# Optimization experiments

Measured on AMD Instinct MI355X. Metric: run time of the kernel, lower is better.

## Reference

```python
import jax, jax.numpy as jnp
import numpy as np

N, MA, F, NF = 512, 64, 128, 16
UPDATE_RATIO = 0.1
DECAY = 1.0
EPS = 1e-12  # avoids NaN grad of sqrt at self-distance 0 (torch diagonal is masked out by exp anyway)


def setup_inputs() -> dict:
    key = jax.random.key(0)
    ks = jax.random.split(key, 8)
    z = jax.random.randint(ks[0], (N, MA), 0, 10, dtype=jnp.int64) if jax.config.jax_enable_x64 else jax.random.randint(ks[0], (N, MA), 0, 10, dtype=jnp.int32)
    # pad last few atoms of each molecule with -1 to exercise the mask
    z = z.at[:, MA - 8:].set(-1)
    r = jax.random.normal(ks[1], (N, MA, 3), dtype=jnp.float32) * 3.0
    h = jax.random.normal(ks[2], (N, MA, F), dtype=jnp.float32)
    distances = jnp.linspace(0.5, 6.0, NF, dtype=jnp.float32)
    widths = jax.random.uniform(ks[3], (NF,), dtype=jnp.float32) * 0.5 + 0.5  # keep sigma > 0
    din = F * (1 + NF)  # 2176
    W1 = jax.random.normal(ks[4], (din, 512), dtype=jnp.float32) * (1.0 / np.sqrt(din))
    b1 = jnp.zeros((512,), dtype=jnp.float32)
    W2 = jax.random.normal(ks[5], (512, F), dtype=jnp.float32) * (1.0 / np.sqrt(512.0))
    b2 = jnp.zeros((F,), dtype=jnp.float32)
    return {"z": z, "r": r, "h": h, "distances": distances, "widths": widths,
            "W1": W1, "b1": b1, "W2": W2, "b2": b2}


def reference(z, r, h, distances, widths, W1, b1, W2, b2):
    n, ma = z.shape
    nf = distances.shape[0]
    # pairwise distance: (n, ma, ma)
    dv = r[:, :, None, :] - r[:, None, :, :]
    d = jnp.sqrt(jnp.sum(dv * dv, axis=-1) + EPS)
    mu = distances.reshape(1, nf, 1, 1)
    sigma = widths.reshape(1, nf, 1, 1)
    mask1 = (z > -1).astype(h.dtype)                      # (n, ma)
    pair_mask = mask1[:, :, None] * mask1[:, None, :]     # (n, ma, ma)
    # Gaussian RBF scores, masked: (n, nf, ma, ma)
    w = pair_mask[:, None] * jnp.exp(-((d[:, None] - mu) ** 2) / sigma) * 5.0
    # aggregate neighbor features: (n, ma, nf, F) -> (n, ma, nf*F)
    u = jnp.einsum('nfab,nbc->nafc', w, h).reshape(n, ma, nf * h.shape[-1])
    v = jnp.concatenate([h, u], axis=2)                   # (n, ma, F*(1+nf))
    v = jax.nn.silu(v @ W1 + b1) @ W2 + b2                # MLP 'net'
    h_new = h + v * UPDATE_RATIO * DECAY * mask1[:, :, None]
    return (z, r, h_new)
```

## Files before the change

### kernel.cpp

```cpp
#include <hip/hip_runtime.h>

#define MA 64
#define F 128
#define NF 16
#define HID 512
#define LDUB 144
#define LDWB 144
#define LDT1B 1040
#define UB0 0
#define UB1 9216
#define WL0 18432
#define WL1 27648

typedef float  float4v __attribute__((ext_vector_type(4)));
typedef short  short8  __attribute__((ext_vector_type(8)));
typedef int    int8v   __attribute__((ext_vector_type(8)));

static __device__ __forceinline__ unsigned int pack2bf(float x, float y) {
    unsigned int a = __float_as_uint(x) + 0x8000u;
    unsigned int b = __float_as_uint(y) + 0x8000u;
    return __builtin_amdgcn_perm(b, a, 0x07060302u);
}
static __device__ __forceinline__ unsigned short f2bf1(float x) {
    return (unsigned short)((__float_as_uint(x) + 0x8000u) >> 16);
}
static __device__ __forceinline__ unsigned int pk4fp8(float a, float b, float c, float d) {
    int p = __builtin_amdgcn_cvt_pk_fp8_f32(a, b, 0, false);
    p = __builtin_amdgcn_cvt_pk_fp8_f32(c, d, p, true);
    return (unsigned int)p;
}

#define LGKM_BAR() do {                                        \
    asm volatile("s_waitcnt lgkmcnt(0)" ::: "memory");         \
    __builtin_amdgcn_s_barrier();                              \
    asm volatile("" ::: "memory");                             \
} while (0)

__global__ void pack_frags(const float* __restrict__ W1, const float* __restrict__ W2,
                           unsigned char* __restrict__ w1p, unsigned short* __restrict__ w2p) {
    int gid  = blockIdx.x * 4 + (threadIdx.x >> 6);
    int lane = threadIdx.x & 63;
    int arow = lane & 15;
    int kq   = lane >> 4;
    if (gid < 544) {
        int kt = gid >> 5, jt = gid & 31;
        const float* base = W1 + (size_t)(kt * 128 + kq * 32) * HID + jt * 16 + arow;
        unsigned int o[8];
        #pragma unroll
        for (int p = 0; p < 8; p++)
            o[p] = pk4fp8(base[(p * 4 + 0) * HID], base[(p * 4 + 1) * HID],
                          base[(p * 4 + 2) * HID], base[(p * 4 + 3) * HID]);
        unsigned char* dst = w1p + ((size_t)gid * 64 + lane) * 32;
        *(uint4*)dst        = (uint4){o[0], o[1], o[2], o[3]};
        *(uint4*)(dst + 16) = (uint4){o[4], o[5], o[6], o[7]};
    } else if (gid < 544 + 128) {
        int g2 = gid - 544;
        int kt = g2 >> 3, mt = g2 & 7;
        const float* base = W2 + (size_t)(kt * 32 + kq * 8) * F + mt * 16 + arow;
        short8 o;
        #pragma unroll
        for (int j = 0; j < 8; j++) o[j] = (short)f2bf1(base[j * F]);
        *(short8*)(w2p + ((size_t)g2 * 64 + lane) * 8) = o;
    }
}

__launch_bounds__(1024, 4)
__global__ void node_conv_mfma(const int* __restrict__ z, const float* __restrict__ rr,
        const float* __restrict__ h, const float* __restrict__ dist,
        const float* __restrict__ wid, const float* __restrict__ b1,
        const float* __restrict__ b2,
        const unsigned char* __restrict__ w1p, const unsigned short* __restrict__ w2p,
        float* __restrict__ out) {
    const int n = blockIdx.x;
    const int tid = threadIdx.x;
    const int lane = tid & 63;
    const int wave = tid >> 6;
    const int arow = lane & 15;
    const int quad = lane >> 4;
    const int kgrp = quad * 8;
    const int whi = wave >> 1;
    const int wlo = wave & 1;

    __shared__ __attribute__((aligned(16))) unsigned char lds[66560];
    __shared__ float r_lds[MA][5];

    const int N = gridDim.x;
    const float* hg = h + (size_t)n * MA * F;

    if (tid < MA) {
        int zi = z[n * MA + tid];
        out[(size_t)n * MA + tid] = (float)zi;
        r_lds[tid][0] = rr[(n * MA + tid) * 3 + 0];
        r_lds[tid][1] = rr[(n * MA + tid) * 3 + 1];
        r_lds[tid][2] = rr[(n * MA + tid) * 3 + 2];
        r_lds[tid][3] = (zi > -1) ? 1.0f : 0.0f;
    }
    if (tid < MA * 3)
        out[(size_t)N * MA + (size_t)n * MA * 3 + tid] = rr[(size_t)n * MA * 3 + tid];

    for (int i = tid; i < MA * F / 4; i += 1024) {
        float4 v = ((const float4*)hg)[i];
        int a = i >> 5, c4 = (i & 31) * 4;
        *(unsigned int*)&lds[UB0 + a * LDUB + c4] = pk4fp8(v.x, v.y, v.z, v.w);
    }
    short8 ah[2];
    {
        int c = whi * 16 + arow;
        #pragma unroll
        for (int ks2 = 0; ks2 < 2; ks2++)
            #pragma unroll
            for (int j = 0; j < 8; j++)
                ah[ks2][j] = (short)f2bf1(hg[(size_t)(ks2 * 32 + kgrp + j) * F + c]);
    }
    __syncthreads();

    const int wa = tid >> 4;
    const int wb0 = (tid & 15) * 4;
    float dpre[4];
    {
        float ax = r_lds[wa][0], ay = r_lds[wa][1], az = r_lds[wa][2];
        float am = r_lds[wa][3];
        #pragma unroll
        for (int j = 0; j < 4; j++) {
            float dx = ax - r_lds[wb0 + j][0];
            float dy = ay - r_lds[wb0 + j][1];
            float dz = az - r_lds[wb0 + j][2];
            float d = sqrtf(dx * dx + dy * dy + dz * dz + 1e-12f);
            float mm = am * r_lds[wb0 + j][3];
            dpre[j] = d + (1.0f - mm) * 1e4f;
        }
    }

    {
        float mu = dist[0];
        float isg = 1.0f / wid[0];
        float e[4];
        #pragma unroll
        for (int j = 0; j < 4; j++) {
            float t = dpre[j] - mu;
            e[j] = 5.0f * __expf(-t * t * isg);
        }
        uint2 wp = { pack2bf(e[0], e[1]), pack2bf(e[2], e[3]) };
        *(uint2*)&lds[WL0 + wa * LDWB + wb0 * 2] = wp;
    }
    int8v afr[2];
    {
        const unsigned char* p0 = w1p + ((size_t)((wave * 2) * 64 + lane)) * 32;
        afr[0] = *(const int8v*)p0;
        afr[1] = *(const int8v*)(p0 + 2048);
    }
    LGKM_BAR();

    const float4v zf = {0.f, 0.f, 0.f, 0.f};
    float4v acc[2][4];
    #pragma unroll
    for (int i = 0; i < 2; i++)
        #pragma unroll
        for (int jv = 0; jv < 4; jv++) acc[i][jv] = zf;

    for (int f = 0; f <= NF; f++) {
        const int sel = f & 1;
        const int ubR = sel ? UB1 : UB0;
        const int ubW = sel ? UB0 : UB1;
        const int wlR = sel ? WL1 : WL0;
        const int wlW = sel ? WL0 : WL1;

        #pragma unroll
        for (int at = 0; at < 4; at++) {
            int8v bfr = *(const int8v*)&lds[ubR + (at * 16 + arow) * LDUB + quad * 32];
            acc[0][at] = __builtin_amdgcn_mfma_scale_f32_16x16x128_f8f6f4(
                afr[0], bfr, acc[0][at], 0, 0, 0, 127, 0, 127);
            acc[1][at] = __builtin_amdgcn_mfma_scale_f32_16x16x128_f8f6f4(
                afr[1], bfr, acc[1][at], 0, 0, 0, 127, 0, 127);
        }

        if (f < NF) {
            const unsigned char* pN = w1p + ((size_t)(((f + 1) * 32 + wave * 2) * 64 + lane)) * 32;
            afr[0] = *(const int8v*)pN;
            afr[1] = *(const int8v*)(pN + 2048);

            float4v ud0 = zf, ud1 = zf;
            #pragma unroll
            for (int ks2 = 0; ks2 < 2; ks2++) {
                short8 bw0 = *(const short8*)&lds[wlR + ((wlo * 2 + 0) * 16 + arow) * LDWB + (ks2 * 32 + kgrp) * 2];
                ud0 = __builtin_amdgcn_mfma_f32_16x16x32_bf16(ah[ks2], bw0, ud0, 0, 0, 0);
                short8 bw1 = *(const short8*)&lds[wlR + ((wlo * 2 + 1) * 16 + arow) * LDWB + (ks2 * 32 + kgrp) * 2];
                ud1 = __builtin_amdgcn_mfma_f32_16x16x32_bf16(ah[ks2], bw1, ud1, 0, 0, 0);
            }
            unsigned int u0 = pk4fp8(ud0[0], ud0[1], ud0[2], ud0[3]);
            unsigned int u1 = pk4fp8(ud1[0], ud1[1], ud1[2], ud1[3]);
            *(unsigned int*)&lds[ubW + ((wlo * 2 + 0) * 16 + arow) * LDUB + whi * 16 + quad * 4] = u0;
            *(unsigned int*)&lds[ubW + ((wlo * 2 + 1) * 16 + arow) * LDUB + whi * 16 + quad * 4] = u1;

            if (f <= NF - 2) {
                float mu = dist[f + 1];
                float isg = 1.0f / wid[f + 1];
                float e[4];
                #pragma unroll
                for (int j = 0; j < 4; j++) {
                    float t = dpre[j] - mu;
                    e[j] = 5.0f * __expf(-t * t * isg);
                }
                uint2 wp = { pack2bf(e[0], e[1]), pack2bf(e[2], e[3]) };
                *(uint2*)&lds[wlW + wa * LDWB + wb0 * 2] = wp;
            }
        }
        LGKM_BAR();
    }

    float4 b1v[2];
    #pragma unroll
    for (int mt = 0; mt < 2; mt++)
        b1v[mt] = *(const float4*)&b1[wave * 32 + mt * 16 + quad * 4];

    #pragma unroll
    for (int mt = 0; mt < 2; mt++) {
        #pragma unroll
        for (int at = 0; at < 4; at++) {
            float xs[4];
            #pragma unroll
            for (int r = 0; r < 4; r++) {
                float x = acc[mt][at][r] + ((const float*)&b1v[mt])[r];
                xs[r] = x / (1.0f + __expf(-x));
            }
            uint2 pv = { pack2bf(xs[0], xs[1]), pack2bf(xs[2], xs[3]) };
            *(uint2*)&lds[(at * 16 + arow) * LDT1B + (wave * 32 + mt * 16 + quad * 4) * 2] = pv;
        }
    }
    LGKM_BAR();

    float4v g2[2] = { zf, zf };

    short8 awA = *(const short8*)(w2p + ((size_t)(whi) * 64 + lane) * 8);
    #pragma unroll
    for (int ks2 = 0; ks2 < 8; ks2++) {
        const int k1 = 2 * ks2 + 1;
        short8 awB = *(const short8*)(w2p + ((size_t)(k1 * 8 + whi) * 64 + lane) * 8);
        #pragma unroll
        for (int j = 0; j < 2; j++) {
            short8 bt = *(const short8*)&lds[((wlo * 2 + j) * 16 + arow) * LDT1B + ((2 * ks2) * 32 + kgrp) * 2];
            g2[j] = __builtin_amdgcn_mfma_f32_16x16x32_bf16(awA, bt, g2[j], 0, 0, 0);
        }
        const int k2 = (ks2 < 7) ? 2 * ks2 + 2 : 0;
        awA = *(const short8*)(w2p + ((size_t)(k2 * 8 + whi) * 64 + lane) * 8);
        #pragma unroll
        for (int j = 0; j < 2; j++) {
            short8 bt = *(const short8*)&lds[((wlo * 2 + j) * 16 + arow) * LDT1B + ((2 * ks2 + 1) * 32 + kgrp) * 2];
            g2[j] = __builtin_amdgcn_mfma_f32_16x16x32_bf16(awB, bt, g2[j], 0, 0, 0);
        }
    }

    float* outh = out + (size_t)N * MA * 4 + (size_t)n * MA * F;
    const int c0 = whi * 16 + quad * 4;
    float4 b2v = *(const float4*)&b2[c0];
    #pragma unroll
    for (int j = 0; j < 2; j++) {
        int a = (wlo * 2 + j) * 16 + arow;
        float m = r_lds[a][3] * 0.1f;
        float4 hv = *(const float4*)&hg[a * F + c0];
        float4 res;
        res.x = hv.x + (g2[j][0] + b2v.x) * m;
        res.y = hv.y + (g2[j][1] + b2v.y) * m;
        res.z = hv.z + (g2[j][2] + b2v.z) * m;
        res.w = hv.w + (g2[j][3] + b2v.w) * m;
        *(float4*)&outh[(size_t)a * F + c0] = res;
    }
}

extern "C" void kernel_launch(void* const* d_in, const int* in_sizes, int n_in,
                              void* d_out, int out_size, void* d_ws, size_t ws_size,
                              hipStream_t stream) {
    const int*   z    = (const int*)d_in[0];
    const float* rr   = (const float*)d_in[1];
    const float* h    = (const float*)d_in[2];
    const float* dist = (const float*)d_in[3];
    const float* wid  = (const float*)d_in[4];
    const float* W1   = (const float*)d_in[5];
    const float* b1   = (const float*)d_in[6];
    const float* W2   = (const float*)d_in[7];
    const float* b2   = (const float*)d_in[8];
    float* out = (float*)d_out;

    int Nmol = in_sizes[0] / MA;

    unsigned char*  w1p = (unsigned char*)d_ws;
    unsigned short* w2p = (unsigned short*)(w1p + (size_t)544 * 64 * 32);

    pack_frags<<<168, 256, 0, stream>>>(W1, W2, w1p, w2p);
    node_conv_mfma<<<Nmol, 1024, 0, stream>>>(z, rr, h, dist, wid, b1, b2, w1p, w2p, out);
}
```

Measured before the change: 144.6 us.

## Retile first MLP GEMM to 4x2 per-wave MFMA tiles with priority hints

Changes each wave's tile of the first-layer FP8 MFMA GEMM from 2 hidden tiles by 4 atom tiles to 4 hidden tiles by 2 atom tiles. Each wave now loads only two LDS B fragments per feature step instead of four, but reads twice as many W1 A fragments from global memory, mid-step. It also wraps the MFMA groups in s_setprio so matrix issue gets priority over other waves. The cost is higher global weight traffic per wave and a second in-loop global load that could stall the MFMA chain.

```diff
diff --git a/kernel.cpp b/kernel.cpp
--- a/kernel.cpp
+++ b/kernel.cpp
@@ -80,6 +80,8 @@
     const int kgrp = quad * 8;
     const int whi = wave >> 1;
     const int wlo = wave & 1;
+    const int jbase = (wave & 7) * 4;
+    const int atb   = (wave >> 3) * 2;
 
     __shared__ __attribute__((aligned(16))) unsigned char lds[66560];
     __shared__ float r_lds[MA][5];
@@ -143,20 +145,20 @@
         uint2 wp = { pack2bf(e[0], e[1]), pack2bf(e[2], e[3]) };
         *(uint2*)&lds[WL0 + wa * LDWB + wb0 * 2] = wp;
     }
-    int8v afr[2];
+    int8v afrA, afrB;
     {
-        const unsigned char* p0 = w1p + ((size_t)((wave * 2) * 64 + lane)) * 32;
-        afr[0] = *(const int8v*)p0;
-        afr[1] = *(const int8v*)(p0 + 2048);
+        const unsigned char* p0 = w1p + ((size_t)(jbase * 64 + lane)) * 32;
+        afrA = *(const int8v*)p0;
+        afrB = *(const int8v*)(p0 + 2048);
     }
     LGKM_BAR();
 
     const float4v zf = {0.f, 0.f, 0.f, 0.f};
-    float4v acc[2][4];
-    #pragma unroll
-    for (int i = 0; i < 2; i++)
-        #pragma unroll
-        for (int jv = 0; jv < 4; jv++) acc[i][jv] = zf;
+    float4v acc[4][2];
+    #pragma unroll
+    for (int i = 0; i < 4; i++)
+        #pragma unroll
+        for (int jv = 0; jv < 2; jv++) acc[i][jv] = zf;
 
     for (int f = 0; f <= NF; f++) {
         const int sel = f & 1;
@@ -164,20 +166,40 @@
         const int ubW = sel ? UB0 : UB1;
         const int wlR = sel ? WL1 : WL0;
         const int wlW = sel ? WL0 : WL1;
-
-        #pragma unroll
-        for (int at = 0; at < 4; at++) {
-            int8v bfr = *(const int8v*)&lds[ubR + (at * 16 + arow) * LDUB + quad * 32];
-            acc[0][at] = __builtin_amdgcn_mfma_scale_f32_16x16x128_f8f6f4(
-                afr[0], bfr, acc[0][at], 0, 0, 0, 127, 0, 127);
-            acc[1][at] = __builtin_amdgcn_mfma_scale_f32_16x16x128_f8f6f4(
-                afr[1], bfr, acc[1][at], 0, 0, 0, 127, 0, 127);
-        }
+        const unsigned char* pseg = w1p + ((size_t)((f * 32 + jbase) * 64 + lane)) * 32;
+
+        int8v bfr0 = *(const int8v*)&lds[ubR + ((atb + 0) * 16 + arow) * LDUB + quad * 32];
+        int8v bfr1 = *(const int8v*)&lds[ubR + ((atb + 1) * 16 + arow) * LDUB + quad * 32];
+
+        __builtin_amdgcn_s_setprio(1);
+        acc[0][0] = __builtin_amdgcn_mfma_scale_f32_16x16x128_f8f6f4(
+            afrA, bfr0, acc[0][0], 0, 0, 0, 127, 0, 127);
+        acc[0][1] = __builtin_amdgcn_mfma_scale_f32_16x16x128_f8f6f4(
+            afrA, bfr1, acc[0][1], 0, 0, 0, 127, 0, 127);
+        acc[1][0] = __builtin_amdgcn_mfma_scale_f32_16x16x128_f8f6f4(
+            afrB, bfr0, acc[1][0], 0, 0, 0, 127, 0, 127);
+        acc[1][1] = __builtin_amdgcn_mfma_scale_f32_16x16x128_f8f6f4(
+            afrB, bfr1, acc[1][1], 0, 0, 0, 127, 0, 127);
+        __builtin_amdgcn_s_setprio(0);
+
+        afrA = *(const int8v*)(pseg + 2 * 2048);
+        afrB = *(const int8v*)(pseg + 3 * 2048);
+
+        __builtin_amdgcn_s_setprio(1);
+        acc[2][0] = __builtin_amdgcn_mfma_scale_f32_16x16x128_f8f6f4(
+            afrA, bfr0, acc[2][0], 0, 0, 0, 127, 0, 127);
+        acc[2][1] = __builtin_amdgcn_mfma_scale_f32_16x16x128_f8f6f4(
+            afrA, bfr1, acc[2][1], 0, 0, 0, 127, 0, 127);
+        acc[3][0] = __builtin_amdgcn_mfma_scale_f32_16x16x128_f8f6f4(
+            afrB, bfr0, acc[3][0], 0, 0, 0, 127, 0, 127);
+        acc[3][1] = __builtin_amdgcn_mfma_scale_f32_16x16x128_f8f6f4(
+            afrB, bfr1, acc[3][1], 0, 0, 0, 127, 0, 127);
+        __builtin_amdgcn_s_setprio(0);
 
         if (f < NF) {
-            const unsigned char* pN = w1p + ((size_t)(((f + 1) * 32 + wave * 2) * 64 + lane)) * 32;
-            afr[0] = *(const int8v*)pN;
-            afr[1] = *(const int8v*)(pN + 2048);
+            const unsigned char* pN = w1p + ((size_t)(((f + 1) * 32 + jbase) * 64 + lane)) * 32;
+            afrA = *(const int8v*)pN;
+            afrB = *(const int8v*)(pN + 2048);
 
             float4v ud0 = zf, ud1 = zf;
             #pragma unroll
@@ -208,23 +230,23 @@
         LGKM_BAR();
     }
 
-    float4 b1v[2];
-    #pragma unroll
-    for (int mt = 0; mt < 2; mt++)
-        b1v[mt] = *(const float4*)&b1[wave * 32 + mt * 16 + quad * 4];
-
-    #pragma unroll
-    for (int mt = 0; mt < 2; mt++) {
-        #pragma unroll
-        for (int at = 0; at < 4; at++) {
+    float4 b1v[4];
+    #pragma unroll
+    for (int mt = 0; mt < 4; mt++)
+        b1v[mt] = *(const float4*)&b1[(jbase + mt) * 16 + quad * 4];
+
+    #pragma unroll
+    for (int mt = 0; mt < 4; mt++) {
+        #pragma unroll
+        for (int i = 0; i < 2; i++) {
             float xs[4];
             #pragma unroll
             for (int r = 0; r < 4; r++) {
-                float x = acc[mt][at][r] + ((const float*)&b1v[mt])[r];
+                float x = acc[mt][i][r] + ((const float*)&b1v[mt])[r];
                 xs[r] = x / (1.0f + __expf(-x));
             }
             uint2 pv = { pack2bf(xs[0], xs[1]), pack2bf(xs[2], xs[3]) };
-            *(uint2*)&lds[(at * 16 + arow) * LDT1B + (wave * 32 + mt * 16 + quad * 4) * 2] = pv;
+            *(uint2*)&lds[((atb + i) * 16 + arow) * LDT1B + ((jbase + mt) * 16 + quad * 4) * 2] = pv;
         }
     }
     LGKM_BAR();
```

Result: slower. 158.6 us (+9.7%).

## Compute RBF weights in registers as MFMA B-fragments instead of via LDS

Applied to the files above, without the earlier changes.

Each wave now precomputes 16 masked pairwise distances that map directly onto its bf16 MFMA B-operand layout. Every filter step it evaluates the Gaussian weights in registers, so the double-buffered weight tile in LDS, its stores and loads, and the one-step-ahead weight computation are gone. The per-wave work split for the neighbor aggregation is remapped: each wave handles one atom tile and two feature tiles, which doubles the h fragments held in registers. The cost is more exp calls per thread (16 instead of 4 per filter) and higher register pressure.

```diff
diff --git a/kernel.cpp b/kernel.cpp
--- a/kernel.cpp
+++ b/kernel.cpp
@@ -5,12 +5,9 @@
 #define NF 16
 #define HID 512
 #define LDUB 144
-#define LDWB 144
 #define LDT1B 1040
 #define UB0 0
 #define UB1 9216
-#define WL0 18432
-#define WL1 27648
 
 typedef float  float4v __attribute__((ext_vector_type(4)));
 typedef short  short8  __attribute__((ext_vector_type(8)));
@@ -80,6 +77,8 @@
     const int kgrp = quad * 8;
     const int whi = wave >> 1;
     const int wlo = wave & 1;
+    const int uat  = wave & 3;
+    const int uct0 = (wave >> 2) * 2;
 
     __shared__ __attribute__((aligned(16))) unsigned char lds[66560];
     __shared__ float r_lds[MA][5];
@@ -103,45 +102,15 @@
         int a = i >> 5, c4 = (i & 31) * 4;
         *(unsigned int*)&lds[UB0 + a * LDUB + c4] = pk4fp8(v.x, v.y, v.z, v.w);
     }
-    short8 ah[2];
-    {
-        int c = whi * 16 + arow;
+    short8 ah2[2][2];
+    #pragma unroll
+    for (int cc = 0; cc < 2; cc++) {
+        int c = (uct0 + cc) * 16 + arow;
         #pragma unroll
         for (int ks2 = 0; ks2 < 2; ks2++)
             #pragma unroll
             for (int j = 0; j < 8; j++)
-                ah[ks2][j] = (short)f2bf1(hg[(size_t)(ks2 * 32 + kgrp + j) * F + c]);
-    }
-    __syncthreads();
-
-    const int wa = tid >> 4;
-    const int wb0 = (tid & 15) * 4;
-    float dpre[4];
-    {
-        float ax = r_lds[wa][0], ay = r_lds[wa][1], az = r_lds[wa][2];
-        float am = r_lds[wa][3];
-        #pragma unroll
-        for (int j = 0; j < 4; j++) {
-            float dx = ax - r_lds[wb0 + j][0];
-            float dy = ay - r_lds[wb0 + j][1];
-            float dz = az - r_lds[wb0 + j][2];
-            float d = sqrtf(dx * dx + dy * dy + dz * dz + 1e-12f);
-            float mm = am * r_lds[wb0 + j][3];
-            dpre[j] = d + (1.0f - mm) * 1e4f;
-        }
-    }
-
-    {
-        float mu = dist[0];
-        float isg = 1.0f / wid[0];
-        float e[4];
-        #pragma unroll
-        for (int j = 0; j < 4; j++) {
-            float t = dpre[j] - mu;
-            e[j] = 5.0f * __expf(-t * t * isg);
-        }
-        uint2 wp = { pack2bf(e[0], e[1]), pack2bf(e[2], e[3]) };
-        *(uint2*)&lds[WL0 + wa * LDWB + wb0 * 2] = wp;
+                ah2[cc][ks2][j] = (short)f2bf1(hg[(size_t)(ks2 * 32 + kgrp + j) * F + c]);
     }
     int8v afr[2];
     {
@@ -149,7 +118,24 @@
         afr[0] = *(const int8v*)p0;
         afr[1] = *(const int8v*)(p0 + 2048);
     }
-    LGKM_BAR();
+    __syncthreads();
+
+    float dpre16[16];
+    {
+        const int athis = uat * 16 + arow;
+        float ax = r_lds[athis][0], ay = r_lds[athis][1], az = r_lds[athis][2];
+        float am = r_lds[athis][3];
+        #pragma unroll
+        for (int i = 0; i < 16; i++) {
+            int bb = (i >> 3) * 32 + kgrp + (i & 7);
+            float dx = ax - r_lds[bb][0];
+            float dy = ay - r_lds[bb][1];
+            float dz = az - r_lds[bb][2];
+            float d = sqrtf(dx * dx + dy * dy + dz * dz + 1e-12f);
+            float mm = am * r_lds[bb][3];
+            dpre16[i] = d + (1.0f - mm) * 1e4f;
+        }
+    }
 
     const float4v zf = {0.f, 0.f, 0.f, 0.f};
     float4v acc[2][4];
@@ -162,8 +148,6 @@
         const int sel = f & 1;
         const int ubR = sel ? UB1 : UB0;
         const int ubW = sel ? UB0 : UB1;
-        const int wlR = sel ? WL1 : WL0;
-        const int wlW = sel ? WL0 : WL1;
 
         #pragma unroll
         for (int at = 0; at < 4; at++) {
@@ -179,30 +163,27 @@
             afr[0] = *(const int8v*)pN;
             afr[1] = *(const int8v*)(pN + 2048);
 
-            float4v ud0 = zf, ud1 = zf;
-            #pragma unroll
-            for (int ks2 = 0; ks2 < 2; ks2++) {
-                short8 bw0 = *(const short8*)&lds[wlR + ((wlo * 2 + 0) * 16 + arow) * LDWB + (ks2 * 32 + kgrp) * 2];
-                ud0 = __builtin_amdgcn_mfma_f32_16x16x32_bf16(ah[ks2], bw0, ud0, 0, 0, 0);
-                short8 bw1 = *(const short8*)&lds[wlR + ((wlo * 2 + 1) * 16 + arow) * LDWB + (ks2 * 32 + kgrp) * 2];
-                ud1 = __builtin_amdgcn_mfma_f32_16x16x32_bf16(ah[ks2], bw1, ud1, 0, 0, 0);
-            }
-            unsigned int u0 = pk4fp8(ud0[0], ud0[1], ud0[2], ud0[3]);
-            unsigned int u1 = pk4fp8(ud1[0], ud1[1], ud1[2], ud1[3]);
-            *(unsigned int*)&lds[ubW + ((wlo * 2 + 0) * 16 + arow) * LDUB + whi * 16 + quad * 4] = u0;
-            *(unsigned int*)&lds[ubW + ((wlo * 2 + 1) * 16 + arow) * LDUB + whi * 16 + quad * 4] = u1;
-
-            if (f <= NF - 2) {
-                float mu = dist[f + 1];
-                float isg = 1.0f / wid[f + 1];
-                float e[4];
+            float mu = dist[f];
+            float isg = 1.0f / wid[f];
+            short8 bwf[2];
+            #pragma unroll
+            for (int ks2 = 0; ks2 < 2; ks2++)
                 #pragma unroll
-                for (int j = 0; j < 4; j++) {
-                    float t = dpre[j] - mu;
-                    e[j] = 5.0f * __expf(-t * t * isg);
+                for (int p = 0; p < 4; p++) {
+                    float t0 = dpre16[ks2 * 8 + 2 * p + 0] - mu;
+                    float t1 = dpre16[ks2 * 8 + 2 * p + 1] - mu;
+                    float e0 = 5.0f * __expf(-t0 * t0 * isg);
+                    float e1 = 5.0f * __expf(-t1 * t1 * isg);
+                    ((unsigned int*)&bwf[ks2])[p] = pack2bf(e0, e1);
                 }
-                uint2 wp = { pack2bf(e[0], e[1]), pack2bf(e[2], e[3]) };
-                *(uint2*)&lds[wlW + wa * LDWB + wb0 * 2] = wp;
+
+            #pragma unroll
+            for (int cc = 0; cc < 2; cc++) {
+                float4v ud = zf;
+                ud = __builtin_amdgcn_mfma_f32_16x16x32_bf16(ah2[cc][0], bwf[0], ud, 0, 0, 0);
+                ud = __builtin_amdgcn_mfma_f32_16x16x32_bf16(ah2[cc][1], bwf[1], ud, 0, 0, 0);
+                unsigned int up = pk4fp8(ud[0], ud[1], ud[2], ud[3]);
+                *(unsigned int*)&lds[ubW + (uat * 16 + arow) * LDUB + (uct0 + cc) * 16 + quad * 4] = up;
             }
         }
         LGKM_BAR();
```

New measurement: 166.4 us. 1.15x slower.

## Switch first MLP GEMM to 32x32x64 FP8 MFMA with repacked W1 fragments

Applied to the files above, without the earlier changes.

Repacks W1 into fragments for the 32x32x64 scaled FP8 MFMA and restructures the per-wave tiling so each wave computes two 32x32 output tiles over half the atoms, instead of eight 16x16 tiles. The U-aggregation work is also reassigned so each wave shares one LDS B-fragment load across two A-fragments. The aim is fewer MFMA issues and fewer LDS fragment reads per filter step. In exchange it loads four W1 fragments per step instead of two and uses a different accumulator and output layout for the SiLU epilogue.

```diff
diff --git a/kernel.cpp b/kernel.cpp
--- a/kernel.cpp
+++ b/kernel.cpp
@@ -12,9 +12,10 @@
 #define WL0 18432
 #define WL1 27648
 
-typedef float  float4v __attribute__((ext_vector_type(4)));
-typedef short  short8  __attribute__((ext_vector_type(8)));
-typedef int    int8v   __attribute__((ext_vector_type(8)));
+typedef float  float4v  __attribute__((ext_vector_type(4)));
+typedef float  float16v __attribute__((ext_vector_type(16)));
+typedef short  short8   __attribute__((ext_vector_type(8)));
+typedef int    int8v    __attribute__((ext_vector_type(8)));
 
 static __device__ __forceinline__ unsigned int pack2bf(float x, float y) {
     unsigned int a = __float_as_uint(x) + 0x8000u;
@@ -40,11 +41,11 @@
                            unsigned char* __restrict__ w1p, unsigned short* __restrict__ w2p) {
     int gid  = blockIdx.x * 4 + (threadIdx.x >> 6);
     int lane = threadIdx.x & 63;
-    int arow = lane & 15;
-    int kq   = lane >> 4;
     if (gid < 544) {
-        int kt = gid >> 5, jt = gid & 31;
-        const float* base = W1 + (size_t)(kt * 128 + kq * 32) * HID + jt * 16 + arow;
+        int kt2 = gid >> 4, jt = gid & 15;
+        int m  = lane & 31;
+        int ks = lane >> 5;
+        const float* base = W1 + (size_t)(kt2 * 64 + ks * 32) * HID + jt * 32 + m;
         unsigned int o[8];
         #pragma unroll
         for (int p = 0; p < 8; p++)
@@ -55,6 +56,8 @@
         *(uint4*)(dst + 16) = (uint4){o[4], o[5], o[6], o[7]};
     } else if (gid < 544 + 128) {
         int g2 = gid - 544;
+        int arow = lane & 15;
+        int kq   = lane >> 4;
         int kt = g2 >> 3, mt = g2 & 7;
         const float* base = W2 + (size_t)(kt * 32 + kq * 8) * F + mt * 16 + arow;
         short8 o;
@@ -78,6 +81,12 @@
     const int arow = lane & 15;
     const int quad = lane >> 4;
     const int kgrp = quad * 8;
+    const int arow31 = lane & 31;
+    const int khalf  = lane >> 5;
+    const int jt0 = (wave & 7) * 2;
+    const int atb = wave >> 3;
+    const int uat  = wave & 3;
+    const int uct0 = (wave >> 2) * 2;
     const int whi = wave >> 1;
     const int wlo = wave & 1;
 
@@ -103,14 +112,15 @@
         int a = i >> 5, c4 = (i & 31) * 4;
         *(unsigned int*)&lds[UB0 + a * LDUB + c4] = pk4fp8(v.x, v.y, v.z, v.w);
     }
-    short8 ah[2];
-    {
-        int c = whi * 16 + arow;
+    short8 ah2[2][2];
+    #pragma unroll
+    for (int cc = 0; cc < 2; cc++) {
+        int c = (uct0 + cc) * 16 + arow;
         #pragma unroll
         for (int ks2 = 0; ks2 < 2; ks2++)
             #pragma unroll
             for (int j = 0; j < 8; j++)
-                ah[ks2][j] = (short)f2bf1(hg[(size_t)(ks2 * 32 + kgrp + j) * F + c]);
+                ah2[cc][ks2][j] = (short)f2bf1(hg[(size_t)(ks2 * 32 + kgrp + j) * F + c]);
     }
     __syncthreads();
 
@@ -143,20 +153,23 @@
         uint2 wp = { pack2bf(e[0], e[1]), pack2bf(e[2], e[3]) };
         *(uint2*)&lds[WL0 + wa * LDWB + wb0 * 2] = wp;
     }
-    int8v afr[2];
+    int8v af00, af01, af10, af11;
     {
-        const unsigned char* p0 = w1p + ((size_t)((wave * 2) * 64 + lane)) * 32;
-        afr[0] = *(const int8v*)p0;
-        afr[1] = *(const int8v*)(p0 + 2048);
+        const unsigned char* p0 = w1p + ((size_t)(0 * 16 + jt0) * 64 + lane) * 32;
+        const unsigned char* p1 = w1p + ((size_t)(1 * 16 + jt0) * 64 + lane) * 32;
+        af00 = *(const int8v*)p0;
+        af10 = *(const int8v*)(p0 + 2048);
+        af01 = *(const int8v*)p1;
+        af11 = *(const int8v*)(p1 + 2048);
     }
     LGKM_BAR();
 
     const float4v zf = {0.f, 0.f, 0.f, 0.f};
-    float4v acc[2][4];
+    float16v acc[2];
     #pragma unroll
     for (int i = 0; i < 2; i++)
         #pragma unroll
-        for (int jv = 0; jv < 4; jv++) acc[i][jv] = zf;
+        for (int r = 0; r < 16; r++) acc[i][r] = 0.f;
 
     for (int f = 0; f <= NF; f++) {
         const int sel = f & 1;
@@ -165,32 +178,39 @@
         const int wlR = sel ? WL1 : WL0;
         const int wlW = sel ? WL0 : WL1;
 
-        #pragma unroll
-        for (int at = 0; at < 4; at++) {
-            int8v bfr = *(const int8v*)&lds[ubR + (at * 16 + arow) * LDUB + quad * 32];
-            acc[0][at] = __builtin_amdgcn_mfma_scale_f32_16x16x128_f8f6f4(
-                afr[0], bfr, acc[0][at], 0, 0, 0, 127, 0, 127);
-            acc[1][at] = __builtin_amdgcn_mfma_scale_f32_16x16x128_f8f6f4(
-                afr[1], bfr, acc[1][at], 0, 0, 0, 127, 0, 127);
+        {
+            const int rowb = ubR + (atb * 32 + arow31) * LDUB + khalf * 32;
+            int8v bfrA = *(const int8v*)&lds[rowb];
+            int8v bfrB = *(const int8v*)&lds[rowb + 64];
+            acc[0] = __builtin_amdgcn_mfma_scale_f32_32x32x64_f8f6f4(
+                af00, bfrA, acc[0], 0, 0, 0, 127, 0, 127);
+            acc[1] = __builtin_amdgcn_mfma_scale_f32_32x32x64_f8f6f4(
+                af10, bfrA, acc[1], 0, 0, 0, 127, 0, 127);
+            acc[0] = __builtin_amdgcn_mfma_scale_f32_32x32x64_f8f6f4(
+                af01, bfrB, acc[0], 0, 0, 0, 127, 0, 127);
+            acc[1] = __builtin_amdgcn_mfma_scale_f32_32x32x64_f8f6f4(
+                af11, bfrB, acc[1], 0, 0, 0, 127, 0, 127);
         }
 
         if (f < NF) {
-            const unsigned char* pN = w1p + ((size_t)(((f + 1) * 32 + wave * 2) * 64 + lane)) * 32;
-            afr[0] = *(const int8v*)pN;
-            afr[1] = *(const int8v*)(pN + 2048);
+            const unsigned char* p0 = w1p + ((size_t)(((f + 1) * 2 + 0) * 16 + jt0) * 64 + lane) * 32;
+            const unsigned char* p1 = w1p + ((size_t)(((f + 1) * 2 + 1) * 16 + jt0) * 64 + lane) * 32;
+            af00 = *(const int8v*)p0;
+            af10 = *(const int8v*)(p0 + 2048);
+            af01 = *(const int8v*)p1;
+            af11 = *(const int8v*)(p1 + 2048);
 
             float4v ud0 = zf, ud1 = zf;
             #pragma unroll
             for (int ks2 = 0; ks2 < 2; ks2++) {
-                short8 bw0 = *(const short8*)&lds[wlR + ((wlo * 2 + 0) * 16 + arow) * LDWB + (ks2 * 32 + kgrp) * 2];
-                ud0 = __builtin_amdgcn_mfma_f32_16x16x32_bf16(ah[ks2], bw0, ud0, 0, 0, 0);
-                short8 bw1 = *(const short8*)&lds[wlR + ((wlo * 2 + 1) * 16 + arow) * LDWB + (ks2 * 32 + kgrp) * 2];
-                ud1 = __builtin_amdgcn_mfma_f32_16x16x32_bf16(ah[ks2], bw1, ud1, 0, 0, 0);
+                short8 bw = *(const short8*)&lds[wlR + (uat * 16 + arow) * LDWB + (ks2 * 32 + kgrp) * 2];
+                ud0 = __builtin_amdgcn_mfma_f32_16x16x32_bf16(ah2[0][ks2], bw, ud0, 0, 0, 0);
+                ud1 = __builtin_amdgcn_mfma_f32_16x16x32_bf16(ah2[1][ks2], bw, ud1, 0, 0, 0);
             }
             unsigned int u0 = pk4fp8(ud0[0], ud0[1], ud0[2], ud0[3]);
             unsigned int u1 = pk4fp8(ud1[0], ud1[1], ud1[2], ud1[3]);
-            *(unsigned int*)&lds[ubW + ((wlo * 2 + 0) * 16 + arow) * LDUB + whi * 16 + quad * 4] = u0;
-            *(unsigned int*)&lds[ubW + ((wlo * 2 + 1) * 16 + arow) * LDUB + whi * 16 + quad * 4] = u1;
+            *(unsigned int*)&lds[ubW + (uat * 16 + arow) * LDUB + (uct0 + 0) * 16 + quad * 4] = u0;
+            *(unsigned int*)&lds[ubW + (uat * 16 + arow) * LDUB + (uct0 + 1) * 16 + quad * 4] = u1;
 
             if (f <= NF - 2) {
                 float mu = dist[f + 1];
@@ -208,23 +228,22 @@
         LGKM_BAR();
     }
 
-    float4 b1v[2];
-    #pragma unroll
-    for (int mt = 0; mt < 2; mt++)
-        b1v[mt] = *(const float4*)&b1[wave * 32 + mt * 16 + quad * 4];
-
-    #pragma unroll
-    for (int mt = 0; mt < 2; mt++) {
-        #pragma unroll
-        for (int at = 0; at < 4; at++) {
+    #pragma unroll
+    for (int jj = 0; jj < 2; jj++) {
+        const int jt = jt0 + jj;
+        const int a  = atb * 32 + arow31;
+        #pragma unroll
+        for (int g = 0; g < 4; g++) {
+            const int jb = jt * 32 + 4 * khalf + 8 * g;
+            float4 b1q = *(const float4*)&b1[jb];
             float xs[4];
             #pragma unroll
-            for (int r = 0; r < 4; r++) {
-                float x = acc[mt][at][r] + ((const float*)&b1v[mt])[r];
-                xs[r] = x / (1.0f + __expf(-x));
+            for (int e = 0; e < 4; e++) {
+                float x = acc[jj][g * 4 + e] + ((const float*)&b1q)[e];
+                xs[e] = x / (1.0f + __expf(-x));
             }
             uint2 pv = { pack2bf(xs[0], xs[1]), pack2bf(xs[2], xs[3]) };
-            *(uint2*)&lds[(at * 16 + arow) * LDT1B + (wave * 32 + mt * 16 + quad * 4) * 2] = pv;
+            *(uint2*)&lds[a * LDT1B + jb * 2] = pv;
         }
     }
     LGKM_BAR();
```

Result: slower. 155.4 us (+7.5%).
